# Optimization experiments

Measured on AMD Instinct MI355X. Metric: run time of the kernel, lower is better.

## Reference

```python
import jax, jax.numpy as jnp
import numpy as np

B, N, FD, H = 8, 256, 1024, 256
RATIO, TEMP = 0.6, 0.5


def setup_inputs() -> dict:
    key = jax.random.key(0)
    ks = jax.random.split(key, 5)
    x = jax.random.normal(ks[0], (B, N, FD), dtype=jnp.float32)
    s1 = 1.0 / np.sqrt(2 * FD)
    W1 = jax.random.uniform(ks[1], (H, 2 * FD), minval=-s1, maxval=s1, dtype=jnp.float32)
    b1 = jax.random.uniform(ks[2], (H,), minval=-s1, maxval=s1, dtype=jnp.float32)
    s2 = 1.0 / np.sqrt(H)
    W2 = jax.random.uniform(ks[3], (1, H), minval=-s2, maxval=s2, dtype=jnp.float32)
    b2 = jax.random.uniform(ks[4], (1,), minval=-s2, maxval=s2, dtype=jnp.float32)
    return {"x": x, "W1": W1, "b1": b1, "W2": W2, "b2": b2}


def reference(x, W1, b1, W2, b2):
    Bb, Nn, Fd = x.shape
    # Linear on cat([row, col]) == row @ W1[:, :F].T + col @ W1[:, F:].T + b1,
    # so project nodes once and broadcast-add instead of materializing [N,N,2F].
    pr = jnp.einsum('bnf,hf->bnh', x, W1[:, :Fd])  # row projections
    pc = jnp.einsum('bnf,hf->bnh', x, W1[:, Fd:])  # col projections
    h = jax.nn.relu(pr[:, :, None, :] + pc[:, None, :, :] + b1)  # [B,N,N,H]
    edge_scores = jnp.einsum('bijh,h->bij', h, W2[0]) + b2[0]    # [B,N,N]
    flat = edge_scores.reshape(Bb, Nn * Nn)
    soft_mask = jax.nn.softmax(flat / TEMP, axis=1)
    k = int(RATIO * Nn * Nn)
    topk_vals, _ = jax.lax.top_k(soft_mask, k)
    threshold = topk_vals[:, -1:]
    causal_mask = jnp.where(soft_mask >= threshold, soft_mask, jnp.zeros_like(soft_mask))
    causal_mask = causal_mask / (causal_mask.sum(axis=1, keepdims=True) + 1e-12)
    conf_mask = 1.0 - causal_mask
    causal_adj = causal_mask.reshape(Bb, Nn, Nn)
    conf_adj = conf_mask.reshape(Bb, Nn, Nn)
    return (causal_adj, conf_adj, edge_scores, soft_mask)
```

## Files before the change

### kernel.cpp

```cpp
#include <hip/hip_runtime.h>

#define BB 8
#define NN 256
#define FDIM 1024
#define HDIM 256
#define NSQ 65536
#define ROWS 2048
#define KSEL 39321
#define NBIN 8192
#define LDSW 72

typedef short s16x8 __attribute__((ext_vector_type(8)));
typedef float f32x4 __attribute__((ext_vector_type(4)));

__device__ __forceinline__ unsigned fkey(float f) {
  unsigned u = __float_as_uint(f);
  return (u & 0x80000000u) ? ~u : (u | 0x80000000u);
}
__device__ __forceinline__ float finv(unsigned k) {
  unsigned u = (k & 0x80000000u) ? (k & 0x7fffffffu) : ~k;
  return __uint_as_float(u);
}
__device__ __forceinline__ unsigned short f2bf(float f) {
  unsigned u = __float_as_uint(f);
  unsigned r = (u + 0x7fffu + ((u >> 16) & 1u)) >> 16;
  return (unsigned short)r;
}

__global__ __launch_bounds__(256) void k_prep(const float* __restrict__ X,
                                              const float* __restrict__ W1,
                                              unsigned short* __restrict__ XB,
                                              unsigned short* __restrict__ W1B,
                                              unsigned* __restrict__ zero) {
  const int bx = blockIdx.x, t = threadIdx.x;
  if (bx < 1280) {
    const float* src = (bx < 1024) ? X : W1;
    unsigned short* dst = (bx < 1024) ? XB : W1B;
    const int idx = ((bx < 1024 ? bx : bx - 1024) * 256 + t) * 8;
    float4 v0 = *(const float4*)&src[idx];
    float4 v1 = *(const float4*)&src[idx + 4];
    s16x8 o;
    o[0] = (short)f2bf(v0.x); o[1] = (short)f2bf(v0.y); o[2] = (short)f2bf(v0.z); o[3] = (short)f2bf(v0.w);
    o[4] = (short)f2bf(v1.x); o[5] = (short)f2bf(v1.y); o[6] = (short)f2bf(v1.z); o[7] = (short)f2bf(v1.w);
    *(s16x8*)&dst[idx] = o;
  } else {
    const int idx = ((bx - 1280) * 256 + t) * 4;
    *(uint4*)&zero[idx] = make_uint4(0u, 0u, 0u, 0u);
  }
}

__global__ __launch_bounds__(256) void k_gemm(const unsigned short* __restrict__ XB,
                                              const unsigned short* __restrict__ W1B,
                                              const float* __restrict__ b1,
                                              float* __restrict__ PRBT,
                                              float* __restrict__ PCT) {
  const int bm = blockIdx.x * 64;
  const int bn = blockIdx.y * 32;
  const int t = threadIdx.x;
  __shared__ short As[64 * LDSW];
  __shared__ short Bs[32 * LDSW];
  const int sr = t >> 2, cg = t & 3;
  const unsigned short* pa = XB + (bm + sr) * FDIM + cg * 16;
  const int srb = t >> 3, cgb = t & 7;
  const unsigned short* pb = (bn < 256)
      ? (W1B + (bn + srb) * (2 * FDIM) + cgb * 8)
      : (W1B + (bn - 256 + srb) * (2 * FDIM) + FDIM + cgb * 8);
  const int w = t >> 6, lane = t & 63;
  const int wm = (w & 1) * 32, wn = (w >> 1) * 16;
  const int q = lane >> 4, m16 = lane & 15;
  f32x4 acc[2] = {};
  s16x8 ra0 = *(const s16x8*)(pa);
  s16x8 ra1 = *(const s16x8*)(pa + 8);
  s16x8 rb = *(const s16x8*)(pb);
  for (int k0 = 0; k0 < FDIM; k0 += 64) {
    __syncthreads();
    *(s16x8*)&As[sr * LDSW + cg * 16]     = ra0;
    *(s16x8*)&As[sr * LDSW + cg * 16 + 8] = ra1;
    *(s16x8*)&Bs[srb * LDSW + cgb * 8]    = rb;
    if (k0 + 64 < FDIM) {
      ra0 = *(const s16x8*)(pa + k0 + 64);
      ra1 = *(const s16x8*)(pa + k0 + 72);
      rb  = *(const s16x8*)(pb + k0 + 64);
    }
    __syncthreads();
#pragma unroll
    for (int koff = 0; koff < 64; koff += 32) {
      s16x8 af0 = *(s16x8*)&As[(wm + m16) * LDSW + koff + q * 8];
      s16x8 af1 = *(s16x8*)&As[(wm + 16 + m16) * LDSW + koff + q * 8];
      s16x8 bf0 = *(s16x8*)&Bs[(wn + m16) * LDSW + koff + q * 8];
      acc[0] = __builtin_amdgcn_mfma_f32_16x16x32_bf16(af0, bf0, acc[0], 0, 0, 0);
      acc[1] = __builtin_amdgcn_mfma_f32_16x16x32_bf16(af1, bf0, acc[1], 0, 0, 0);
    }
  }
#pragma unroll
  for (int rt = 0; rt < 2; ++rt) {
    const int hn = bn + wn + m16;
    const int row0 = bm + wm + rt * 16 + q * 4;
    if (hn < 256) {
      const float bias = b1[hn];
      float4 v = make_float4(acc[rt][0] + bias, acc[rt][1] + bias,
                             acc[rt][2] + bias, acc[rt][3] + bias);
      *(float4*)&PRBT[hn * ROWS + row0] = v;
    } else {
      float4 v = make_float4(acc[rt][0], acc[rt][1], acc[rt][2], acc[rt][3]);
      *(float4*)&PCT[(hn - 256) * ROWS + row0] = v;
    }
  }
}

__global__ __launch_bounds__(512) void k_edge(const float* __restrict__ PRBT,
                                              const float* __restrict__ PCT,
                                              const float* __restrict__ W2,
                                              const float* __restrict__ b2,
                                              float* __restrict__ edge,
                                              unsigned* __restrict__ gcount,
                                              float* __restrict__ gvsum) {
  const int b = blockIdx.z;
  const int i0 = blockIdx.y * 64, j0 = blockIdx.x * 32;
  const int t = threadIdx.x;
  __shared__ float prs[64][68];
  __shared__ float pcs[64][36];
  __shared__ float w2s[HDIM];
  __shared__ unsigned lhc[NBIN / 2];
  __shared__ float lhv[NBIN];
  if (t < HDIM) w2s[t] = W2[t];
#pragma unroll
  for (int i = 0; i < 2; ++i) ((uint4*)lhc)[t + i * 512] = make_uint4(0u, 0u, 0u, 0u);
#pragma unroll
  for (int i = 0; i < 4; ++i) ((float4*)lhv)[t + i * 512] = make_float4(0.f, 0.f, 0.f, 0.f);
  const float bias = b2[0];
  const int tmi = t >> 4, tnj = t & 15;
  float acc[2][2] = {};
  for (int h0 = 0; h0 < HDIM; h0 += 64) {
    __syncthreads();
#pragma unroll
    for (int s = 0; s < 2; ++s) {
      int idx = t + s * 512;
      int hh = idx >> 4, ig = idx & 15;
      *(float4*)&prs[hh][ig * 4] =
          *(const float4*)&PRBT[(h0 + hh) * ROWS + b * NN + i0 + ig * 4];
    }
    {
      int hh = t >> 3, jg = t & 7;
      *(float4*)&pcs[hh][jg * 4] =
          *(const float4*)&PCT[(h0 + hh) * ROWS + b * NN + j0 + jg * 4];
    }
    __syncthreads();
#pragma unroll 8
    for (int h = 0; h < 64; ++h) {
      const float w = w2s[h0 + h];
      const float2 a = *(const float2*)&prs[h][tmi * 2];
      const float2 c = *(const float2*)&pcs[h][tnj * 2];
      acc[0][0] += fmaxf(a.x + c.x, 0.f) * w;
      acc[0][1] += fmaxf(a.x + c.y, 0.f) * w;
      acc[1][0] += fmaxf(a.y + c.x, 0.f) * w;
      acc[1][1] += fmaxf(a.y + c.y, 0.f) * w;
    }
  }
  const int ibase = i0 + tmi * 2, jbase = j0 + tnj * 2;
#pragma unroll
  for (int i = 0; i < 2; ++i) {
    float2 v = make_float2(acc[i][0] + bias, acc[i][1] + bias);
    *(float2*)&edge[b * NSQ + (ibase + i) * NN + jbase] = v;
    float ex = __expf(v.x * 2.f), ey = __expf(v.y * 2.f);
    unsigned bx = fkey(v.x) >> 19, by = fkey(v.y) >> 19;
    atomicAdd(&lhc[bx >> 1], 1u << ((bx & 1) * 16));
    atomicAdd(&lhv[bx], ex);
    atomicAdd(&lhc[by >> 1], 1u << ((by & 1) * 16));
    atomicAdd(&lhv[by], ey);
  }
  __syncthreads();
  unsigned* gc = gcount + b * NBIN;
  float* gv = gvsum + b * NBIN;
#pragma unroll
  for (int i = 0; i < 8; ++i) {
    const int idx = t + i * 512;
    unsigned wv = lhc[idx];
    if (wv) {
      unsigned lo = wv & 0xFFFFu, hi = wv >> 16;
      if (lo) atomicAdd(&gc[2 * idx], lo);
      if (hi) atomicAdd(&gc[2 * idx + 1], hi);
    }
  }
#pragma unroll
  for (int i = 0; i < 16; ++i) {
    const int idx = t + i * 512;
    float vv = lhv[idx];
    if (vv != 0.f) atomicAdd(&gv[idx], vv);
  }
}

__global__ __launch_bounds__(256) void k_out(const float* __restrict__ edge,
                                             const unsigned* __restrict__ gcount,
                                             const float* __restrict__ gvsum,
                                             float* __restrict__ soft,
                                             float* __restrict__ causal,
                                             float* __restrict__ conf) {
  const int b = blockIdx.y;
  const int t = threadIdx.x;
  __shared__ unsigned S[256];
  __shared__ float V[256];
  __shared__ unsigned ou[1];
  __shared__ float of[3];
  const unsigned* hc = gcount + b * NBIN;
  const float* hv = gvsum + b * NBIN;
  unsigned cs = 0; float vs = 0.f;
  for (int i = 0; i < 32; ++i) { cs += hc[t * 32 + i]; vs += hv[t * 32 + i]; }
  S[t] = cs; V[t] = vs;
  __syncthreads();
  for (int off = 1; off < 256; off <<= 1) {
    unsigned su = (t + off < 256) ? S[t + off] : 0u;
    float vu = (t + off < 256) ? V[t + off] : 0.f;
    __syncthreads();
    S[t] += su; V[t] += vu;
    __syncthreads();
  }
  if (t == 0) of[2] = V[0];
  const int above = (int)(S[t] - cs);
  if (above < KSEL && (int)S[t] >= KSEL) {
    int cum = above;
    float vcum = V[t] - vs;
    for (int i = 31; i >= 0; --i) {
      unsigned c = hc[t * 32 + i];
      float v = hv[t * 32 + i];
      cum += (int)c;
      if (cum >= KSEL) { ou[0] = (unsigned)(t * 32 + i); of[0] = vcum; of[1] = v; break; }
      vcum += v;
    }
  }
  __syncthreads();
  const float th = finv(ou[0] << 19);
  const float Z = of[2];
  const float invZ = 1.f / Z;
  const float msum = (of[0] + of[1]) * invZ;
  const float invD = 1.f / (msum + 1e-12f);
  const int off = b * NSQ + blockIdx.x * 2048 + t * 8;
#pragma unroll
  for (int i = 0; i < 8; i += 4) {
    float4 v = *(const float4*)&edge[off + i];
    float4 o = make_float4(__expf(v.x * 2.f) * invZ, __expf(v.y * 2.f) * invZ,
                           __expf(v.z * 2.f) * invZ, __expf(v.w * 2.f) * invZ);
    *(float4*)&soft[off + i] = o;
    float cx = v.x >= th ? o.x * invD : 0.f;
    float cy = v.y >= th ? o.y * invD : 0.f;
    float cz = v.z >= th ? o.z * invD : 0.f;
    float cw = v.w >= th ? o.w * invD : 0.f;
    *(float4*)&causal[off + i] = make_float4(cx, cy, cz, cw);
    *(float4*)&conf[off + i]   = make_float4(1.f - cx, 1.f - cy, 1.f - cz, 1.f - cw);
  }
}

extern "C" void kernel_launch(void* const* d_in, const int* in_sizes, int n_in,
                              void* d_out, int out_size, void* d_ws, size_t ws_size,
                              hipStream_t stream) {
  const float* x  = (const float*)d_in[0];
  const float* W1 = (const float*)d_in[1];
  const float* b1 = (const float*)d_in[2];
  const float* W2 = (const float*)d_in[3];
  const float* b2 = (const float*)d_in[4];

  float* out = (float*)d_out;
  float* causal = out;
  float* conf   = out + 1 * 524288;
  float* edge   = out + 2 * 524288;
  float* soft   = out + 3 * 524288;

  float* ws = (float*)d_ws;
  float*          PRBT   = ws;
  float*          PCT    = ws + 524288;
  unsigned short* XB     = (unsigned short*)(ws + 1048576);
  unsigned short* W1B    = (unsigned short*)(ws + 2097152);
  unsigned*       gcount = (unsigned*)(ws + 2359296);
  float*          gvsum  = (float*)(ws + 2424832);

  k_prep<<<1408, 256, 0, stream>>>(x, W1, XB, W1B, gcount);
  k_gemm<<<dim3(32, 16), 256, 0, stream>>>(XB, W1B, b1, PRBT, PCT);
  k_edge<<<dim3(8, 4, 8), 512, 0, stream>>>(PRBT, PCT, W2, b2, edge, gcount, gvsum);
  k_out<<<dim3(32, 8), 256, 0, stream>>>(edge, gcount, gvsum, soft, causal, conf);
}
```

Before: 106.7 us.

## Double-buffer LDS in projection GEMM with 64x64 tiles; vectorize histogram loads

The projection GEMM now uses a 64x64 output tile per block with two LDS buffers. The next K-slice is stored into the alternate buffer while the MFMAs read the current one, which drops one barrier per iteration and doubles per-wave MFMA work (2x2 accumulators). The grid halves to 256 blocks, which may cut occupancy and parallelism on a GPU with many CUs. Separately, the histogram prefix in the output kernel now reads its bins with 128-bit vector loads instead of scalar loops.

```diff
diff --git a/kernel.cpp b/kernel.cpp
--- a/kernel.cpp
+++ b/kernel.cpp
@@ -55,55 +55,74 @@
                                               float* __restrict__ PRBT,
                                               float* __restrict__ PCT) {
   const int bm = blockIdx.x * 64;
-  const int bn = blockIdx.y * 32;
+  const int bn = blockIdx.y * 64;
   const int t = threadIdx.x;
-  __shared__ short As[64 * LDSW];
-  __shared__ short Bs[32 * LDSW];
+  __shared__ short As[2][64 * LDSW];
+  __shared__ short Bs[2][64 * LDSW];
   const int sr = t >> 2, cg = t & 3;
   const unsigned short* pa = XB + (bm + sr) * FDIM + cg * 16;
-  const int srb = t >> 3, cgb = t & 7;
   const unsigned short* pb = (bn < 256)
-      ? (W1B + (bn + srb) * (2 * FDIM) + cgb * 8)
-      : (W1B + (bn - 256 + srb) * (2 * FDIM) + FDIM + cgb * 8);
+      ? (W1B + (bn + sr) * (2 * FDIM) + cg * 16)
+      : (W1B + (bn - 256 + sr) * (2 * FDIM) + FDIM + cg * 16);
   const int w = t >> 6, lane = t & 63;
-  const int wm = (w & 1) * 32, wn = (w >> 1) * 16;
+  const int wm = (w & 1) * 32, wn = (w >> 1) * 32;
   const int q = lane >> 4, m16 = lane & 15;
-  f32x4 acc[2] = {};
+  f32x4 acc[2][2] = {};
   s16x8 ra0 = *(const s16x8*)(pa);
   s16x8 ra1 = *(const s16x8*)(pa + 8);
-  s16x8 rb = *(const s16x8*)(pb);
+  s16x8 rb0 = *(const s16x8*)(pb);
+  s16x8 rb1 = *(const s16x8*)(pb + 8);
+  *(s16x8*)&As[0][sr * LDSW + cg * 16]     = ra0;
+  *(s16x8*)&As[0][sr * LDSW + cg * 16 + 8] = ra1;
+  *(s16x8*)&Bs[0][sr * LDSW + cg * 16]     = rb0;
+  *(s16x8*)&Bs[0][sr * LDSW + cg * 16 + 8] = rb1;
+  ra0 = *(const s16x8*)(pa + 64);
+  ra1 = *(const s16x8*)(pa + 72);
+  rb0 = *(const s16x8*)(pb + 64);
+  rb1 = *(const s16x8*)(pb + 72);
+  __syncthreads();
+  int cur = 0;
   for (int k0 = 0; k0 < FDIM; k0 += 64) {
-    __syncthreads();
-    *(s16x8*)&As[sr * LDSW + cg * 16]     = ra0;
-    *(s16x8*)&As[sr * LDSW + cg * 16 + 8] = ra1;
-    *(s16x8*)&Bs[srb * LDSW + cgb * 8]    = rb;
     if (k0 + 64 < FDIM) {
-      ra0 = *(const s16x8*)(pa + k0 + 64);
-      ra1 = *(const s16x8*)(pa + k0 + 72);
-      rb  = *(const s16x8*)(pb + k0 + 64);
-    }
-    __syncthreads();
+      *(s16x8*)&As[cur ^ 1][sr * LDSW + cg * 16]     = ra0;
+      *(s16x8*)&As[cur ^ 1][sr * LDSW + cg * 16 + 8] = ra1;
+      *(s16x8*)&Bs[cur ^ 1][sr * LDSW + cg * 16]     = rb0;
+      *(s16x8*)&Bs[cur ^ 1][sr * LDSW + cg * 16 + 8] = rb1;
+      if (k0 + 128 < FDIM) {
+        ra0 = *(const s16x8*)(pa + k0 + 128);
+        ra1 = *(const s16x8*)(pa + k0 + 136);
+        rb0 = *(const s16x8*)(pb + k0 + 128);
+        rb1 = *(const s16x8*)(pb + k0 + 136);
+      }
+    }
 #pragma unroll
     for (int koff = 0; koff < 64; koff += 32) {
-      s16x8 af0 = *(s16x8*)&As[(wm + m16) * LDSW + koff + q * 8];
-      s16x8 af1 = *(s16x8*)&As[(wm + 16 + m16) * LDSW + koff + q * 8];
-      s16x8 bf0 = *(s16x8*)&Bs[(wn + m16) * LDSW + koff + q * 8];
-      acc[0] = __builtin_amdgcn_mfma_f32_16x16x32_bf16(af0, bf0, acc[0], 0, 0, 0);
-      acc[1] = __builtin_amdgcn_mfma_f32_16x16x32_bf16(af1, bf0, acc[1], 0, 0, 0);
-    }
-  }
-#pragma unroll
-  for (int rt = 0; rt < 2; ++rt) {
-    const int hn = bn + wn + m16;
-    const int row0 = bm + wm + rt * 16 + q * 4;
-    if (hn < 256) {
-      const float bias = b1[hn];
-      float4 v = make_float4(acc[rt][0] + bias, acc[rt][1] + bias,
-                             acc[rt][2] + bias, acc[rt][3] + bias);
-      *(float4*)&PRBT[hn * ROWS + row0] = v;
-    } else {
-      float4 v = make_float4(acc[rt][0], acc[rt][1], acc[rt][2], acc[rt][3]);
-      *(float4*)&PCT[(hn - 256) * ROWS + row0] = v;
+      s16x8 af0 = *(s16x8*)&As[cur][(wm + m16) * LDSW + koff + q * 8];
+      s16x8 af1 = *(s16x8*)&As[cur][(wm + 16 + m16) * LDSW + koff + q * 8];
+      s16x8 bf0 = *(s16x8*)&Bs[cur][(wn + m16) * LDSW + koff + q * 8];
+      s16x8 bf1 = *(s16x8*)&Bs[cur][(wn + 16 + m16) * LDSW + koff + q * 8];
+      acc[0][0] = __builtin_amdgcn_mfma_f32_16x16x32_bf16(af0, bf0, acc[0][0], 0, 0, 0);
+      acc[0][1] = __builtin_amdgcn_mfma_f32_16x16x32_bf16(af0, bf1, acc[0][1], 0, 0, 0);
+      acc[1][0] = __builtin_amdgcn_mfma_f32_16x16x32_bf16(af1, bf0, acc[1][0], 0, 0, 0);
+      acc[1][1] = __builtin_amdgcn_mfma_f32_16x16x32_bf16(af1, bf1, acc[1][1], 0, 0, 0);
+    }
+    __syncthreads();
+    cur ^= 1;
+  }
+#pragma unroll
+  for (int am = 0; am < 2; ++am) {
+#pragma unroll
+    for (int bq = 0; bq < 2; ++bq) {
+      const int hn = bn + wn + bq * 16 + m16;
+      const int row0 = bm + wm + am * 16 + q * 4;
+      f32x4 a = acc[am][bq];
+      if (hn < 256) {
+        const float bias = b1[hn];
+        *(float4*)&PRBT[hn * ROWS + row0] =
+            make_float4(a[0] + bias, a[1] + bias, a[2] + bias, a[3] + bias);
+      } else {
+        *(float4*)&PCT[(hn - 256) * ROWS + row0] = make_float4(a[0], a[1], a[2], a[3]);
+      }
     }
   }
 }
@@ -205,7 +224,17 @@
   const unsigned* hc = gcount + b * NBIN;
   const float* hv = gvsum + b * NBIN;
   unsigned cs = 0; float vs = 0.f;
-  for (int i = 0; i < 32; ++i) { cs += hc[t * 32 + i]; vs += hv[t * 32 + i]; }
+  {
+    const uint4* hc4 = (const uint4*)(hc + t * 32);
+    const float4* hv4 = (const float4*)(hv + t * 32);
+#pragma unroll
+    for (int i = 0; i < 8; ++i) {
+      uint4 c = hc4[i];
+      float4 v = hv4[i];
+      cs += c.x + c.y + c.z + c.w;
+      vs += v.x + v.y + v.z + v.w;
+    }
+  }
   S[t] = cs; V[t] = vs;
   __syncthreads();
   for (int off = 1; off < 256; off <<= 1) {
@@ -274,7 +303,7 @@
   float*          gvsum  = (float*)(ws + 2424832);
 
   k_prep<<<1408, 256, 0, stream>>>(x, W1, XB, W1B, gcount);
-  k_gemm<<<dim3(32, 16), 256, 0, stream>>>(XB, W1B, b1, PRBT, PCT);
+  k_gemm<<<dim3(32, 8), 256, 0, stream>>>(XB, W1B, b1, PRBT, PCT);
   k_edge<<<dim3(8, 4, 8), 512, 0, stream>>>(PRBT, PCT, W2, b2, edge, gcount, gvsum);
   k_out<<<dim3(32, 8), 256, 0, stream>>>(edge, gcount, gvsum, soft, causal, conf);
 }
```

New measurement: 108.8 us. About the same (+2.0%).

## Fuse edge scoring and softmax/top-k output via cooperative grid sync

Applied to the files above, without the earlier changes.

Merges the edge-score kernel and the output kernel into one cooperative launch that does a grid-wide sync after the global histogram is built. Each block then computes the threshold from the histogram itself and writes soft, causal and conf for its own tile from scores kept in registers, so edge is no longer re-read from memory. This removes one kernel launch and one pass over edge. In exchange it adds cooperative-launch overhead and a grid barrier, makes every one of the 256 blocks scan the histogram redundantly, and replaces float4 stores with float2 stores.

```diff
diff --git a/kernel.cpp b/kernel.cpp
--- a/kernel.cpp
+++ b/kernel.cpp
@@ -1,4 +1,7 @@
 #include <hip/hip_runtime.h>
+#include <hip/hip_cooperative_groups.h>
+
+namespace cg = cooperative_groups;
 
 #define BB 8
 #define NN 256
@@ -108,13 +111,16 @@
   }
 }
 
-__global__ __launch_bounds__(512) void k_edge(const float* __restrict__ PRBT,
-                                              const float* __restrict__ PCT,
-                                              const float* __restrict__ W2,
-                                              const float* __restrict__ b2,
-                                              float* __restrict__ edge,
-                                              unsigned* __restrict__ gcount,
-                                              float* __restrict__ gvsum) {
+__global__ __launch_bounds__(512) void k_edge_out(const float* __restrict__ PRBT,
+                                                  const float* __restrict__ PCT,
+                                                  const float* __restrict__ W2,
+                                                  const float* __restrict__ b2,
+                                                  float* __restrict__ edge,
+                                                  unsigned* __restrict__ gcount,
+                                                  float* __restrict__ gvsum,
+                                                  float* __restrict__ soft,
+                                                  float* __restrict__ causal,
+                                                  float* __restrict__ conf) {
   const int b = blockIdx.z;
   const int i0 = blockIdx.y * 64, j0 = blockIdx.x * 32;
   const int t = threadIdx.x;
@@ -123,6 +129,10 @@
   __shared__ float w2s[HDIM];
   __shared__ unsigned lhc[NBIN / 2];
   __shared__ float lhv[NBIN];
+  __shared__ unsigned S[256];
+  __shared__ float V[256];
+  __shared__ unsigned ou[1];
+  __shared__ float of[3];
   if (t < HDIM) w2s[t] = W2[t];
 #pragma unroll
   for (int i = 0; i < 2; ++i) ((uint4*)lhc)[t + i * 512] = make_uint4(0u, 0u, 0u, 0u);
@@ -158,9 +168,11 @@
     }
   }
   const int ibase = i0 + tmi * 2, jbase = j0 + tnj * 2;
+  float vsave[2][2];
 #pragma unroll
   for (int i = 0; i < 2; ++i) {
     float2 v = make_float2(acc[i][0] + bias, acc[i][1] + bias);
+    vsave[i][0] = v.x; vsave[i][1] = v.y;
     *(float2*)&edge[b * NSQ + (ibase + i) * NN + jbase] = v;
     float ex = __expf(v.x * 2.f), ey = __expf(v.y * 2.f);
     unsigned bx = fkey(v.x) >> 19, by = fkey(v.y) >> 19;
@@ -188,65 +200,63 @@
     float vv = lhv[idx];
     if (vv != 0.f) atomicAdd(&gv[idx], vv);
   }
-}
-
-__global__ __launch_bounds__(256) void k_out(const float* __restrict__ edge,
-                                             const unsigned* __restrict__ gcount,
-                                             const float* __restrict__ gvsum,
-                                             float* __restrict__ soft,
-                                             float* __restrict__ causal,
-                                             float* __restrict__ conf) {
-  const int b = blockIdx.y;
-  const int t = threadIdx.x;
-  __shared__ unsigned S[256];
-  __shared__ float V[256];
-  __shared__ unsigned ou[1];
-  __shared__ float of[3];
+  cg::this_grid().sync();
   const unsigned* hc = gcount + b * NBIN;
   const float* hv = gvsum + b * NBIN;
   unsigned cs = 0; float vs = 0.f;
-  for (int i = 0; i < 32; ++i) { cs += hc[t * 32 + i]; vs += hv[t * 32 + i]; }
-  S[t] = cs; V[t] = vs;
+  if (t < 256) {
+    const uint4* hc4 = (const uint4*)(hc + t * 32);
+    const float4* hv4 = (const float4*)(hv + t * 32);
+#pragma unroll
+    for (int i = 0; i < 8; ++i) {
+      uint4 c = hc4[i];
+      float4 v = hv4[i];
+      cs += c.x + c.y + c.z + c.w;
+      vs += v.x + v.y + v.z + v.w;
+    }
+    S[t] = cs; V[t] = vs;
+  }
   __syncthreads();
   for (int off = 1; off < 256; off <<= 1) {
-    unsigned su = (t + off < 256) ? S[t + off] : 0u;
-    float vu = (t + off < 256) ? V[t + off] : 0.f;
-    __syncthreads();
-    S[t] += su; V[t] += vu;
+    unsigned su = 0u; float vu = 0.f;
+    if (t < 256) {
+      su = (t + off < 256) ? S[t + off] : 0u;
+      vu = (t + off < 256) ? V[t + off] : 0.f;
+    }
+    __syncthreads();
+    if (t < 256) { S[t] += su; V[t] += vu; }
     __syncthreads();
   }
   if (t == 0) of[2] = V[0];
-  const int above = (int)(S[t] - cs);
-  if (above < KSEL && (int)S[t] >= KSEL) {
-    int cum = above;
-    float vcum = V[t] - vs;
-    for (int i = 31; i >= 0; --i) {
-      unsigned c = hc[t * 32 + i];
-      float v = hv[t * 32 + i];
-      cum += (int)c;
-      if (cum >= KSEL) { ou[0] = (unsigned)(t * 32 + i); of[0] = vcum; of[1] = v; break; }
-      vcum += v;
+  if (t < 256) {
+    const int above = (int)(S[t] - cs);
+    if (above < KSEL && (int)S[t] >= KSEL) {
+      int cum = above;
+      float vcum = V[t] - vs;
+      for (int i = 31; i >= 0; --i) {
+        unsigned c = hc[t * 32 + i];
+        float v = hv[t * 32 + i];
+        cum += (int)c;
+        if (cum >= KSEL) { ou[0] = (unsigned)(t * 32 + i); of[0] = vcum; of[1] = v; break; }
+        vcum += v;
+      }
     }
   }
   __syncthreads();
   const float th = finv(ou[0] << 19);
-  const float Z = of[2];
-  const float invZ = 1.f / Z;
+  const float invZ = 1.f / of[2];
   const float msum = (of[0] + of[1]) * invZ;
   const float invD = 1.f / (msum + 1e-12f);
-  const int off = b * NSQ + blockIdx.x * 2048 + t * 8;
-#pragma unroll
-  for (int i = 0; i < 8; i += 4) {
-    float4 v = *(const float4*)&edge[off + i];
-    float4 o = make_float4(__expf(v.x * 2.f) * invZ, __expf(v.y * 2.f) * invZ,
-                           __expf(v.z * 2.f) * invZ, __expf(v.w * 2.f) * invZ);
-    *(float4*)&soft[off + i] = o;
-    float cx = v.x >= th ? o.x * invD : 0.f;
-    float cy = v.y >= th ? o.y * invD : 0.f;
-    float cz = v.z >= th ? o.z * invD : 0.f;
-    float cw = v.w >= th ? o.w * invD : 0.f;
-    *(float4*)&causal[off + i] = make_float4(cx, cy, cz, cw);
-    *(float4*)&conf[off + i]   = make_float4(1.f - cx, 1.f - cy, 1.f - cz, 1.f - cw);
+#pragma unroll
+  for (int i = 0; i < 2; ++i) {
+    const int off = b * NSQ + (ibase + i) * NN + jbase;
+    float ox = __expf(vsave[i][0] * 2.f) * invZ;
+    float oy = __expf(vsave[i][1] * 2.f) * invZ;
+    *(float2*)&soft[off] = make_float2(ox, oy);
+    float cx = vsave[i][0] >= th ? ox * invD : 0.f;
+    float cy = vsave[i][1] >= th ? oy * invD : 0.f;
+    *(float2*)&causal[off] = make_float2(cx, cy);
+    *(float2*)&conf[off]   = make_float2(1.f - cx, 1.f - cy);
   }
 }
 
@@ -275,6 +285,11 @@
 
   k_prep<<<1408, 256, 0, stream>>>(x, W1, XB, W1B, gcount);
   k_gemm<<<dim3(32, 16), 256, 0, stream>>>(XB, W1B, b1, PRBT, PCT);
-  k_edge<<<dim3(8, 4, 8), 512, 0, stream>>>(PRBT, PCT, W2, b2, edge, gcount, gvsum);
-  k_out<<<dim3(32, 8), 256, 0, stream>>>(edge, gcount, gvsum, soft, causal, conf);
-}
+
+  const float* PRBTc = PRBT; const float* PCTc = PCT;
+  void* args[] = {(void*)&PRBTc, (void*)&PCTc, (void*)&W2, (void*)&b2,
+                  (void*)&edge, (void*)&gcount, (void*)&gvsum,
+                  (void*)&soft, (void*)&causal, (void*)&conf};
+  hipLaunchCooperativeKernel((const void*)k_edge_out, dim3(8, 4, 8), dim3(512),
+                             args, 0, stream);
+}
```

Measured after the change: 139.5 us. 30.8% more time.
